# Optimization experiments

Hardware: AMD Instinct MI355X
Metric: run time of the kernel (lower is better)

Reference implementation:

```python
import jax, jax.numpy as jnp
import numpy as np

B, C, H, W = 4, 256, 64, 64
CH = C // 2  # inner channels


def setup_inputs() -> dict:
    key = jax.random.key(0)
    ks = jax.random.split(key, 9)
    s = 1.0 / np.sqrt(C)
    so = 1.0 / np.sqrt(CH)
    return {
        "x": jax.random.normal(ks[0], (B, C, H, W), dtype=jnp.float32),
        "teta_w": jax.random.uniform(ks[1], (CH, C), jnp.float32, -s, s),
        "teta_b": jax.random.uniform(ks[2], (CH,), jnp.float32, -s, s),
        "fi_w": jax.random.uniform(ks[3], (CH, C), jnp.float32, -s, s),
        "fi_b": jax.random.uniform(ks[4], (CH,), jnp.float32, -s, s),
        "gi_w": jax.random.uniform(ks[5], (CH, C), jnp.float32, -s, s),
        "gi_b": jax.random.uniform(ks[6], (CH,), jnp.float32, -s, s),
        "out_w": jax.random.uniform(ks[7], (C, CH), jnp.float32, -so, so),
        "out_b": jax.random.uniform(ks[8], (C,), jnp.float32, -so, so),
    }


def _conv1x1(x, w, b):
    # x: (B, Cin, H, W), w: (Cout, Cin) -> (B, Cout, H, W)
    return jnp.einsum('bchw,oc->bohw', x, w) + b[None, :, None, None]


def reference(x, teta_w, teta_b, fi_w, fi_b, gi_w, gi_b, out_w, out_b):
    b, c, h, w = x.shape
    n = h * w
    ch = teta_w.shape[0]
    # NOTE: original uses .view (reshape), NOT transpose, to get (B, N, Ch)
    x1 = _conv1x1(x, teta_w, teta_b).reshape(b, ch, n).reshape(b, n, ch)
    x2 = _conv1x1(x, fi_w, fi_b).reshape(b, ch, n)            # (B, Ch, N)
    x3 = _conv1x1(x, gi_w, gi_b).reshape(b, ch, n).reshape(b, n, ch)
    # softmax over dim=1 (rows), as in the original
    attn = jax.nn.softmax(jnp.matmul(x1, x2), axis=1)          # (B, N, N)
    y = jnp.matmul(attn, x3)                                   # (B, N, Ch)
    y = jnp.swapaxes(y, 1, 2).reshape(b, ch, h, w)
    return x + _conv1x1(y, out_w, out_b)
```

## Files before the change

### kernel.cpp

```cpp
#include <hip/hip_runtime.h>
#include <hip/hip_bf16.h>

#define BB 4
#define CC 256
#define CHH 128
#define NN 4096
#define KSHIFT 12.0f

typedef __attribute__((ext_vector_type(8))) short bf16x8;
typedef __attribute__((ext_vector_type(4))) float f32x4;

__device__ __forceinline__ float to_f(float v) { return v; }
__device__ __forceinline__ float to_f(__hip_bfloat16 v) { return __bfloat162float(v); }
__device__ __forceinline__ void st_f(float* p, float v) { *p = v; }
__device__ __forceinline__ void st_f(__hip_bfloat16* p, float v) { *p = __float2bfloat16(v); }
__device__ __forceinline__ unsigned short f2bf(float f) {
    __hip_bfloat16 h = __float2bfloat16(f);
    unsigned short u;
    __builtin_memcpy(&u, &h, 2);
    return u;
}
__device__ __forceinline__ bf16x8 ldb8(const unsigned short* p) { return *(const bf16x8*)p; }

__device__ __forceinline__ void gload_lds16(const unsigned short* g, unsigned short* l) {
    __builtin_amdgcn_global_load_lds(
        (const __attribute__((address_space(1))) unsigned int*)g,
        (__attribute__((address_space(3))) unsigned int*)l, 16, 0, 0);
}

__device__ __forceinline__ int detect_flag_block(const void* tb, int* sflag) {
    int tid = threadIdx.x;
    if (tid < 64) {
        const __hip_bfloat16* p = (const __hip_bfloat16*)tb;
        int big = 0, zero_even = 0;
#pragma unroll
        for (int k = 0; k < 2; ++k) {
            int idx = tid * 2 + k;
            float v = __bfloat162float(p[idx]);
            if (!(fabsf(v) <= 0.5f)) big = 1;
            if ((idx & 1) == 0 && v == 0.0f) zero_even = 1;
        }
        unsigned long long bigm = __ballot(big);
        unsigned long long zm = __ballot(zero_even);
        if (tid == 0) *sflag = (bigm != 0ULL || __popcll(zm) >= 32) ? 1 : 0;
    }
    __syncthreads();
    return *sflag;
}

template <typename T>
__device__ __forceinline__ void prep_body(const T* tw, const T* fw, const T* gw, const T* ow,
                                          const T* tb2, const T* fb, const T* gb, const T* ob,
                                          unsigned short* Wb, unsigned short* OWb,
                                          float* Bf, float* OBf) {
    int idx = blockIdx.x * 256 + threadIdx.x;
    if (idx < 98304) {
        int cv = idx >> 15, rem = idx & 32767;
        const T* src = cv == 0 ? tw : (cv == 1 ? fw : gw);
        Wb[idx] = f2bf(to_f(src[rem]));
    } else if (idx < 131072) {
        OWb[idx - 98304] = f2bf(to_f(ow[idx - 98304]));
    } else if (idx < 131456) {
        int r = idx - 131072;
        int cv = r >> 7, j = r & 127;
        const T* src = cv == 0 ? tb2 : (cv == 1 ? fb : gb);
        Bf[r] = to_f(src[j]);
    } else if (idx < 131712) {
        OBf[idx - 131456] = to_f(ob[idx - 131456]);
    }
}

template <typename T>
__device__ __forceinline__ void xtrans_body(const T* __restrict__ x, unsigned short* __restrict__ xt,
                                            int id, unsigned short (*t)[68]) {
    int b = id >> 8;
    const T* in = x + (size_t)b * CC * NN;
    unsigned short* out = xt + (size_t)b * NN * CC;
    int p0 = (id & 63) * 64, c0 = ((id >> 6) & 3) * 64;
    int flat = threadIdx.x;
#pragma unroll
    for (int tt = 0; tt < 16; ++tt) {
        int idd = flat + tt * 256;
        int rr = idd >> 6, cc = idd & 63;
        t[cc][rr] = f2bf(to_f(in[(size_t)(c0 + rr) * NN + p0 + cc]));
    }
    __syncthreads();
#pragma unroll
    for (int tt = 0; tt < 16; ++tt) {
        int idd = flat + tt * 256;
        int pp = idd >> 6, jj = idd & 63;
        out[(size_t)(p0 + pp) * CC + c0 + jj] = t[pp][jj];
    }
}

__launch_bounds__(256)
__global__ void prep_xtrans_kernel(const void* x,
                                   const void* tw, const void* fw, const void* gw, const void* ow,
                                   const void* tb2, const void* fb, const void* gb, const void* ob,
                                   unsigned short* Wb, unsigned short* OWb,
                                   float* Bf, float* OBf,
                                   unsigned short* __restrict__ xt) {
    __shared__ int sflag;
    __shared__ unsigned short t[64][68];
    int flag = detect_flag_block(tb2, &sflag);
    if (blockIdx.x < 515) {
        if (flag)
            prep_body<float>((const float*)tw, (const float*)fw, (const float*)gw, (const float*)ow,
                             (const float*)tb2, (const float*)fb, (const float*)gb, (const float*)ob,
                             Wb, OWb, Bf, OBf);
        else
            prep_body<__hip_bfloat16>((const __hip_bfloat16*)tw, (const __hip_bfloat16*)fw,
                                      (const __hip_bfloat16*)gw, (const __hip_bfloat16*)ow,
                                      (const __hip_bfloat16*)tb2, (const __hip_bfloat16*)fb,
                                      (const __hip_bfloat16*)gb, (const __hip_bfloat16*)ob,
                                      Wb, OWb, Bf, OBf);
    } else {
        int id = blockIdx.x - 515;
        if (flag) xtrans_body<float>((const float*)x, xt, id, t);
        else      xtrans_body<__hip_bfloat16>((const __hip_bfloat16*)x, xt, id, t);
    }
}

__launch_bounds__(256)
__global__ void conv3_mfma_kernel(const unsigned short* __restrict__ xt,
                                  const unsigned short* __restrict__ Wb,
                                  const float* __restrict__ Bf,
                                  unsigned short* __restrict__ T1b,
                                  unsigned short* __restrict__ T2t,
                                  unsigned short* __restrict__ T3b) {
    int b = blockIdx.y;
    int p0 = blockIdx.x * 16;
    int flat = threadIdx.x;
    int w = flat >> 6, lane = flat & 63, m = lane & 15, quad = lane >> 4;
    const unsigned short* xrow = xt + ((size_t)b * NN + p0 + m) * CC;
    bf16x8 xf[8];
#pragma unroll
    for (int kc = 0; kc < 8; ++kc)
        xf[kc] = ldb8(&xrow[kc * 32 + quad * 8]);
    unsigned short* t1  = T1b + (size_t)b * CHH * NN;
    unsigned short* t2t = T2t + (size_t)b * CHH * NN;
    unsigned short* t3  = T3b + (size_t)b * CHH * NN;
#pragma unroll
    for (int q = 0; q < 6; ++q) {
        int t = w * 6 + q;
        int cv = t >> 3, ot = t & 7;
        int o0 = ot * 16;
        const unsigned short* wrow = Wb + ((size_t)cv * CHH + o0 + m) * CC;
        f32x4 acc = {0.f, 0.f, 0.f, 0.f};
        __builtin_amdgcn_s_setprio(1);
#pragma unroll
        for (int kc = 0; kc < 8; ++kc) {
            bf16x8 wf = ldb8(&wrow[kc * 32 + quad * 8]);
            acc = __builtin_amdgcn_mfma_f32_16x16x32_bf16(wf, xf[kc], acc, 0, 0, 0);
        }
        __builtin_amdgcn_s_setprio(0);
        unsigned short hv[4];
#pragma unroll
        for (int r = 0; r < 4; ++r)
            hv[r] = f2bf(acc[r] + Bf[cv * CHH + o0 + quad * 4 + r]);
        if (cv == 1) {
            unsigned int lo = (unsigned int)hv[0] | ((unsigned int)hv[1] << 16);
            unsigned int hi = (unsigned int)hv[2] | ((unsigned int)hv[3] << 16);
            int src = (lane & 3) * 16 + (lane >> 2);
            unsigned int tlo = (unsigned int)__shfl((int)lo, src, 64);
            unsigned int thi = (unsigned int)__shfl((int)hi, src, 64);
            unsigned int* dst = (unsigned int*)&t2t[(size_t)(p0 + (lane >> 2)) * CHH +
                                                    o0 + (lane & 3) * 4];
            dst[0] = tlo;
            dst[1] = thi;
        } else {
            unsigned short* outp = (cv == 0) ? t1 : t3;
#pragma unroll
            for (int r = 0; r < 4; ++r)
                outp[(size_t)(o0 + quad * 4 + r) * NN + p0 + m] = hv[r];
        }
    }
}

__launch_bounds__(256)
__global__ void trans_stats_kernel(const unsigned short* __restrict__ T1b,
                                   const unsigned short* __restrict__ T2t,
                                   const unsigned short* __restrict__ T3b,
                                   unsigned short* __restrict__ X3t,
                                   float* __restrict__ Lpart) {
    __shared__ unsigned short arena[2 * 64 * 128];
    int flat = threadIdx.x;
    if (blockIdx.x >= 1024) {
        int id = blockIdx.x - 1024;
        int bz = id >> 7;
        int by = (id >> 1) & 63;
        int bx = id & 1;
        const unsigned short* in = T3b + (size_t)bz * NN * CHH;
        unsigned short* out = X3t + (size_t)bz * NN * CHH;
        int c0 = bx * 64, r0 = by * 64;
        unsigned short (*t)[68] = (unsigned short (*)[68])arena;
#pragma unroll
        for (int tt = 0; tt < 16; ++tt) {
            int id2 = flat + tt * 256;
            int r = id2 >> 6, c = id2 & 63;
            t[c][r] = in[(size_t)(r0 + r) * CHH + c0 + c];
        }
        __syncthreads();
#pragma unroll
        for (int tt = 0; tt < 16; ++tt) {
            int id2 = flat + tt * 256;
            int c = id2 >> 6, r = id2 & 63;
            out[(size_t)(c0 + c) * NN + r0 + r] = t[c][r];
        }
        return;
    }
    int blk = blockIdx.x;
    int b = (blk & 7) >> 1;
    int rest = (blk >> 3) * 2 + (blk & 1);
    int strip = rest >> 3, iq = rest & 7;
    int ibase = iq * 512;
    int w = flat >> 6, lane = flat & 63, m = lane & 15, quad = lane >> 4;
    const unsigned short* A  = T1b + (size_t)b * CHH * NN;
    const unsigned short* Bt = T2t + (size_t)b * CHH * NN;

    int u0w = strip * 128 + w * 32;
    bf16x8 bfr[2][4];
#pragma unroll
    for (int g = 0; g < 2; ++g)
#pragma unroll
        for (int kc = 0; kc < 4; ++kc)
            bfr[g][kc] = ldb8(&Bt[(size_t)(u0w + g * 16 + m) * CHH + kc * 32 + quad * 8]);

#define STAGE_TH(dst, ii)                                                          \
    _Pragma("unroll")                                                              \
    for (int i_ = 0; i_ < 4; ++i_) {                                               \
        int sl = i_ * 256 + flat;                                                  \
        int r_ = sl >> 4, ch_ = sl & 15;                                           \
        int c_ = ch_ ^ (r_ & 7);                                                   \
        gload_lds16(&A[(size_t)((ii) + r_) * CHH + c_ * 8],                        \
                    arena + (dst) * 8192 + sl * 8);                                \
    }

    float csum[2] = {0.f, 0.f};
    STAGE_TH(0, ibase);
    __syncthreads();
    int cur = 0;
    for (int t = 0; t < 8; ++t) {
        if (t < 7) { STAGE_TH(cur ^ 1, ibase + (t + 1) * 64); }
        const unsigned short* thc = arena + cur * 8192;
#pragma unroll
        for (int s = 0; s < 4; ++s) {
            int irow = s * 16 + m;
            bf16x8 af[4];
#pragma unroll
            for (int kc = 0; kc < 4; ++kc) {
                int ch = (kc * 4 + quad) ^ (irow & 7);
                af[kc] = *(const bf16x8*)&thc[irow * 128 + ch * 8];
            }
            __builtin_amdgcn_s_setprio(1);
#pragma unroll
            for (int g = 0; g < 2; ++g) {
                f32x4 acc = {0.f, 0.f, 0.f, 0.f};
#pragma unroll
                for (int kc = 0; kc < 4; ++kc)
                    acc = __builtin_amdgcn_mfma_f32_16x16x32_bf16(af[kc], bfr[g][kc], acc, 0, 0, 0);
#pragma unroll
                for (int r = 0; r < 4; ++r)
                    csum[g] += __expf(acc[r] - KSHIFT);
            }
            __builtin_amdgcn_s_setprio(0);
        }
        if (t < 7) {
            __syncthreads();
            cur ^= 1;
        }
    }
#undef STAGE_TH
#pragma unroll
    for (int g = 0; g < 2; ++g) {
        csum[g] += __shfl_xor(csum[g], 16, 64);
        csum[g] += __shfl_xor(csum[g], 32, 64);
        if (lane < 16)
            Lpart[((size_t)iq * BB + b) * NN + u0w + g * 16 + m] = csum[g];
    }
}

__launch_bounds__(512, 2)
__global__ void attn_mfma_kernel(const unsigned short* __restrict__ T1b,
                                 const unsigned short* __restrict__ T2t,
                                 const unsigned short* __restrict__ X3t,
                                 const float* __restrict__ Lpart,
                                 unsigned short* __restrict__ Yp0,
                                 unsigned short* __restrict__ Yp1,
                                 unsigned short* __restrict__ Yp2,
                                 unsigned short* __restrict__ Yp3) {
    int blk = blockIdx.x;
    int b = (blk & 7) >> 1;
    int rest = (blk >> 3) * 2 + (blk & 1);
    int it = rest >> 2, uc = rest & 3;
    int i0 = it * 128;
    unsigned short* Yp = uc == 0 ? Yp0 : (uc == 1 ? Yp1 : (uc == 2 ? Yp2 : Yp3));
    int flat = threadIdx.x;
    int w = flat >> 6, lane = flat & 63, m = lane & 15, quad = lane >> 4;
    int ig = w & 3, h = w >> 2;
    const unsigned short* A  = T1b + (size_t)b * CHH * NN;
    const unsigned short* Bt = T2t + (size_t)b * CHH * NN;
    const unsigned short* X3 = X3t + (size_t)b * CHH * NN;

    __shared__ __align__(16) unsigned char smem[69632];
    unsigned short* bt0 = (unsigned short*)smem;
    unsigned short* x3s = (unsigned short*)(smem + 32768);
    unsigned short* pTg = (unsigned short*)(smem + 49152) + ig * 2048;
    float* llh = (float*)(smem + 65536);

    int ubeg = uc * 1024;
#pragma unroll
    for (int k = 0; k < 2; ++k) {
        int idx = k * 512 + flat;
        int u = ubeg + idx;
        float s = 0.f;
#pragma unroll
        for (int c = 0; c < 8; ++c)
            s += Lpart[((size_t)c * BB + b) * NN + u];
        llh[idx] = __logf(s) + KSHIFT;
    }

    int iw = i0 + ig * 32;
    int j0 = h * 64;
    bf16x8 ath[2][4];
#pragma unroll
    for (int g = 0; g < 2; ++g)
#pragma unroll
        for (int kc = 0; kc < 4; ++kc)
            ath[g][kc] = ldb8(&A[(size_t)(iw + g * 16 + m) * CHH + kc * 32 + quad * 8]);
    f32x4 yacc[2][4];
#pragma unroll
    for (int g = 0; g < 2; ++g)
#pragma unroll
        for (int js = 0; js < 4; ++js) yacc[g][js] = (f32x4){0.f, 0.f, 0.f, 0.f};

#define STAGE_BT(dst, uu)                                                          \
    _Pragma("unroll")                                                              \
    for (int i_ = 0; i_ < 2; ++i_) {                                    \
        int sl = i_ * 512 + flat;                                                  \
        int u_ = sl >> 4, ch_ = sl & 15;                                           \
        int c_ = ch_ ^ (u_ & 7);                                                   \
        gload_lds16(&Bt[(size_t)((uu) + u_) * CHH + c_ * 8],                       \
                    bt0 + (dst) * 8192 + sl * 8);                                  \
    }
#define STAGE_X3(uu)                                                               \
    _Pragma("unroll")                                                              \
    for (int i_ = 0; i_ < 2; ++i_) {                                    \
        int sl = i_ * 512 + flat;                                                  \
        int j_ = sl >> 3, ch_ = sl & 7;                                            \
        int c_ = ch_ ^ (j_ & 7);                                                   \
        gload_lds16(&X3[(size_t)j_ * NN + (uu) + c_ * 8], x3s + sl * 8);           \
    }

    STAGE_BT(0, ubeg);
    STAGE_X3(ubeg);
    __syncthreads();
    int cur = 0;
    for (int t = 0; t < 16; ++t) {
        int u0 = ubeg + t * 64;
        if (t < 15) { STAGE_BT(cur ^ 1, u0 + 64); }
        const unsigned short* btc = bt0 + cur * 8192;
#pragma unroll
        for (int su = 0; su < 2; ++su) {
            int ul = h * 32 + su * 16 + m;
            f32x4 a0 = {0.f, 0.f, 0.f, 0.f}, a1 = {0.f, 0.f, 0.f, 0.f};
            __builtin_amdgcn_s_setprio(1);
#pragma unroll
            for (int kc = 0; kc < 4; ++kc) {
                int ch = (kc * 4 + quad) ^ (ul & 7);
                bf16x8 bf = *(const bf16x8*)&btc[ul * 128 + ch * 8];
                a0 = __builtin_amdgcn_mfma_f32_16x16x32_bf16(bf, ath[0][kc], a0, 0, 0, 0);
                a1 = __builtin_amdgcn_mfma_f32_16x16x32_bf16(bf, ath[1][kc], a1, 0, 0, 0);
            }
            __builtin_amdgcn_s_setprio(0);
            int ubase = h * 32 + su * 16 + quad * 4;
            int lb = t * 64 + ubase;
            unsigned int p00 = (unsigned int)f2bf(__expf(a0[0] - llh[lb + 0])) |
                               ((unsigned int)f2bf(__expf(a0[1] - llh[lb + 1])) << 16);
            unsigned int p01 = (unsigned int)f2bf(__expf(a0[2] - llh[lb + 2])) |
                               ((unsigned int)f2bf(__expf(a0[3] - llh[lb + 3])) << 16);
            unsigned int p10 = (unsigned int)f2bf(__expf(a1[0] - llh[lb + 0])) |
                               ((unsigned int)f2bf(__expf(a1[1] - llh[lb + 1])) << 16);
            unsigned int p11 = (unsigned int)f2bf(__expf(a1[2] - llh[lb + 2])) |
                               ((unsigned int)f2bf(__expf(a1[3] - llh[lb + 3])) << 16);
            int chs = ((ubase >> 3) ^ (m & 7)) * 8 + (ubase & 7);
            unsigned int* d0 = (unsigned int*)&pTg[m * 64 + chs];
            d0[0] = p00; d0[1] = p01;
            unsigned int* d1 = (unsigned int*)&pTg[(16 + m) * 64 + chs];
            d1[0] = p10; d1[1] = p11;
        }
        __syncthreads();
#pragma unroll
        for (int ku = 0; ku < 2; ++ku) {
            bf16x8 pa0 = *(const bf16x8*)&pTg[m * 64 + ((ku * 4 + quad) ^ (m & 7)) * 8];
            bf16x8 pa1 = *(const bf16x8*)&pTg[(16 + m) * 64 + ((ku * 4 + quad) ^ (m & 7)) * 8];
            __builtin_amdgcn_s_setprio(1);
#pragma unroll
            for (int js = 0; js < 4; ++js) {
                int j = j0 + js * 16 + m;
                int ch = (ku * 4 + quad) ^ (j & 7);
                bf16x8 xb = *(const bf16x8*)&x3s[j * 64 + ch * 8];
                yacc[0][js] = __builtin_amdgcn_mfma_f32_16x16x32_bf16(pa0, xb, yacc[0][js], 0, 0, 0);
                yacc[1][js] = __builtin_amdgcn_mfma_f32_16x16x32_bf16(pa1, xb, yacc[1][js], 0, 0, 0);
            }
            __builtin_amdgcn_s_setprio(0);
        }
        __syncthreads();
        if (t < 15) { STAGE_X3(u0 + 64); }
        cur ^= 1;
    }
#undef STAGE_BT
#undef STAGE_X3
#pragma unroll
    for (int g = 0; g < 2; ++g)
#pragma unroll
        for (int js = 0; js < 4; ++js)
#pragma unroll
            for (int r = 0; r < 4; ++r)
                Yp[((size_t)b * NN + iw + g * 16 + quad * 4 + r) * CHH +
                   j0 + js * 16 + m] = f2bf(yacc[g][js][r]);
}

template <typename T>
__device__ __forceinline__ void outconv_body(const T* __restrict__ x,
                                             const unsigned short* __restrict__ Yp0,
                                             const unsigned short* __restrict__ Yp1,
                                             const unsigned short* __restrict__ Yp2,
                                             const unsigned short* __restrict__ Yp3,
                                             const unsigned short* __restrict__ OWb,
                                             const float* __restrict__ OBf,
                                             T* __restrict__ out) {
    int b = blockIdx.y;
    int p0 = blockIdx.x * 16;
    int flat = threadIdx.x;
    int w = flat >> 6, lane = flat & 63, m = lane & 15, quad = lane >> 4;
    size_t yoff = ((size_t)b * NN + p0 + m) * CHH;
    const unsigned short* yrows[4] = {Yp0 + yoff, Yp1 + yoff, Yp2 + yoff, Yp3 + yoff};
    bf16x8 yf[4][4];
#pragma unroll
    for (int pz = 0; pz < 4; ++pz)
#pragma unroll
        for (int kc = 0; kc < 4; ++kc)
            yf[pz][kc] = ldb8(&yrows[pz][kc * 32 + quad * 8]);
#pragma unroll
    for (int q = 0; q < 4; ++q) {
        int o0 = (w * 4 + q) * 16;
        const unsigned short* wrow = OWb + (size_t)(o0 + m) * CHH;
        f32x4 acc = {0.f, 0.f, 0.f, 0.f};
        __builtin_amdgcn_s_setprio(1);
#pragma unroll
        for (int kc = 0; kc < 4; ++kc) {
            bf16x8 aw = ldb8(&wrow[kc * 32 + quad * 8]);
#pragma unroll
            for (int pz = 0; pz < 4; ++pz)
                acc = __builtin_amdgcn_mfma_f32_16x16x32_bf16(aw, yf[pz][kc], acc, 0, 0, 0);
        }
        __builtin_amdgcn_s_setprio(0);
#pragma unroll
        for (int r = 0; r < 4; ++r) {
            int co = o0 + quad * 4 + r;
            size_t oi = ((size_t)b * CC + co) * NN + p0 + m;
            st_f(&out[oi], acc[r] + OBf[co] + to_f(x[oi]));
        }
    }
}

__launch_bounds__(256)
__global__ void outconv_mfma_kernel(const void* x, const void* tb2,
                                    const unsigned short* __restrict__ Yp0,
                                    const unsigned short* __restrict__ Yp1,
                                    const unsigned short* __restrict__ Yp2,
                                    const unsigned short* __restrict__ Yp3,
                                    const unsigned short* __restrict__ OWb,
                                    const float* __restrict__ OBf,
                                    void* out) {
    __shared__ int sflag;
    int flag = detect_flag_block(tb2, &sflag);
    if (flag)
        outconv_body<float>((const float*)x, Yp0, Yp1, Yp2, Yp3, OWb, OBf, (float*)out);
    else
        outconv_body<__hip_bfloat16>((const __hip_bfloat16*)x, Yp0, Yp1, Yp2, Yp3, OWb, OBf,
                                     (__hip_bfloat16*)out);
}

extern "C" void kernel_launch(void* const* d_in, const int* in_sizes, int n_in,
                              void* d_out, int out_size, void* d_ws, size_t ws_size,
                              hipStream_t stream) {
    const void* x  = d_in[0];
    const void* tw = d_in[1];
    const void* tb = d_in[2];
    const void* fw = d_in[3];
    const void* fb = d_in[4];
    const void* gw = d_in[5];
    const void* gb = d_in[6];
    const void* ow = d_in[7];
    const void* ob = d_in[8];

    const size_t TE = (size_t)BB * CHH * NN;
    unsigned short* T1b = (unsigned short*)d_ws;
    unsigned short* T2t = T1b + TE;
    unsigned short* X3t = T2t + TE;
    unsigned short* T3b = X3t + TE;
    unsigned short* xt  = T3b + TE;
    unsigned short* Yp0 = xt;
    unsigned short* Yp1 = xt + TE;
    unsigned short* Yp2 = T3b;
    unsigned short* Yp3 = xt + 2 * TE;
    unsigned short* Wb  = Yp3 + TE;
    unsigned short* OWb = Wb + 98304;
    float* Bf    = (float*)(OWb + 32768);
    float* OBf   = Bf + 384;
    float* Lpart = OBf + 256;

    prep_xtrans_kernel<<<dim3(1539), 256, 0, stream>>>(x, tw, fw, gw, ow, tb, fb, gb, ob,
                                                       Wb, OWb, Bf, OBf, xt);
    conv3_mfma_kernel<<<dim3(NN / 16, BB), 256, 0, stream>>>(xt, Wb, Bf, T1b, T2t, T3b);
    trans_stats_kernel<<<dim3(1536), 256, 0, stream>>>(T1b, T2t, T3b, X3t, Lpart);
    attn_mfma_kernel<<<dim3(512), 512, 0, stream>>>(T1b, T2t, X3t, Lpart, Yp0, Yp1, Yp2, Yp3);
    outconv_mfma_kernel<<<dim3(NN / 16, BB), 256, 0, stream>>>(x, tb, Yp0, Yp1, Yp2, Yp3,
                                                               OWb, OBf, d_out);
}
```

Before: 193.4 us.

## Fuse x transpose into conv3 kernel and switch softmax to exp2 domain

```diff
diff --git a/kernel.cpp b/kernel.cpp
--- a/kernel.cpp
+++ b/kernel.cpp
@@ -5,7 +5,8 @@
 #define CC 256
 #define CHH 128
 #define NN 4096
-#define KSHIFT 12.0f
+#define KSHIFT2 17.312340490667562f
+#define LOG2E 1.4426950408889634f
 
 typedef __attribute__((ext_vector_type(8))) short bf16x8;
 typedef __attribute__((ext_vector_type(4))) float f32x4;
@@ -28,6 +29,24 @@
         (__attribute__((address_space(3))) unsigned int*)l, 16, 0, 0);
 }
 
+__device__ __forceinline__ void load16(const __hip_bfloat16* src, unsigned short* v) {
+    bf16x8 a = *(const bf16x8*)src;
+    bf16x8 b = *(const bf16x8*)(src + 8);
+#pragma unroll
+    for (int k = 0; k < 8; ++k) {
+        v[k] = ((unsigned short*)&a)[k];
+        v[8 + k] = ((unsigned short*)&b)[k];
+    }
+}
+__device__ __forceinline__ void load16(const float* src, unsigned short* v) {
+#pragma unroll
+    for (int q = 0; q < 4; ++q) {
+        f32x4 f = *(const f32x4*)(src + q * 4);
+#pragma unroll
+        for (int k = 0; k < 4; ++k) v[q * 4 + k] = f2bf(f[k]);
+    }
+}
+
 __device__ __forceinline__ int detect_flag_block(const void* tb, int* sflag) {
     int tid = threadIdx.x;
     if (tid < 64) {
@@ -57,93 +76,73 @@
     if (idx < 98304) {
         int cv = idx >> 15, rem = idx & 32767;
         const T* src = cv == 0 ? tw : (cv == 1 ? fw : gw);
-        Wb[idx] = f2bf(to_f(src[rem]));
+        float v = to_f(src[rem]);
+        if (cv == 1) v *= LOG2E;
+        Wb[idx] = f2bf(v);
     } else if (idx < 131072) {
         OWb[idx - 98304] = f2bf(to_f(ow[idx - 98304]));
     } else if (idx < 131456) {
         int r = idx - 131072;
         int cv = r >> 7, j = r & 127;
         const T* src = cv == 0 ? tb2 : (cv == 1 ? fb : gb);
-        Bf[r] = to_f(src[j]);
+        float v = to_f(src[j]);
+        if (cv == 1) v *= LOG2E;
+        Bf[r] = v;
     } else if (idx < 131712) {
         OBf[idx - 131456] = to_f(ob[idx - 131456]);
     }
 }
 
+__launch_bounds__(256)
+__global__ void prep_kernel(const void* tw, const void* fw, const void* gw, const void* ow,
+                            const void* tb2, const void* fb, const void* gb, const void* ob,
+                            unsigned short* Wb, unsigned short* OWb, float* Bf, float* OBf) {
+    __shared__ int sflag;
+    int flag = detect_flag_block(tb2, &sflag);
+    if (flag)
+        prep_body<float>((const float*)tw, (const float*)fw, (const float*)gw, (const float*)ow,
+                         (const float*)tb2, (const float*)fb, (const float*)gb, (const float*)ob,
+                         Wb, OWb, Bf, OBf);
+    else
+        prep_body<__hip_bfloat16>((const __hip_bfloat16*)tw, (const __hip_bfloat16*)fw,
+                                  (const __hip_bfloat16*)gw, (const __hip_bfloat16*)ow,
+                                  (const __hip_bfloat16*)tb2, (const __hip_bfloat16*)fb,
+                                  (const __hip_bfloat16*)gb, (const __hip_bfloat16*)ob,
+                                  Wb, OWb, Bf, OBf);
+}
+
 template <typename T>
-__device__ __forceinline__ void xtrans_body(const T* __restrict__ x, unsigned short* __restrict__ xt,
-                                            int id, unsigned short (*t)[68]) {
-    int b = id >> 8;
-    const T* in = x + (size_t)b * CC * NN;
-    unsigned short* out = xt + (size_t)b * NN * CC;
-    int p0 = (id & 63) * 64, c0 = ((id >> 6) & 3) * 64;
-    int flat = threadIdx.x;
-#pragma unroll
-    for (int tt = 0; tt < 16; ++tt) {
-        int idd = flat + tt * 256;
-        int rr = idd >> 6, cc = idd & 63;
-        t[cc][rr] = f2bf(to_f(in[(size_t)(c0 + rr) * NN + p0 + cc]));
-    }
-    __syncthreads();
-#pragma unroll
-    for (int tt = 0; tt < 16; ++tt) {
-        int idd = flat + tt * 256;
-        int pp = idd >> 6, jj = idd & 63;
-        out[(size_t)(p0 + pp) * CC + c0 + jj] = t[pp][jj];
-    }
-}
-
-__launch_bounds__(256)
-__global__ void prep_xtrans_kernel(const void* x,
-                                   const void* tw, const void* fw, const void* gw, const void* ow,
-                                   const void* tb2, const void* fb, const void* gb, const void* ob,
-                                   unsigned short* Wb, unsigned short* OWb,
-                                   float* Bf, float* OBf,
-                                   unsigned short* __restrict__ xt) {
-    __shared__ int sflag;
-    __shared__ unsigned short t[64][68];
-    int flag = detect_flag_block(tb2, &sflag);
-    if (blockIdx.x < 515) {
-        if (flag)
-            prep_body<float>((const float*)tw, (const float*)fw, (const float*)gw, (const float*)ow,
-                             (const float*)tb2, (const float*)fb, (const float*)gb, (const float*)ob,
-                             Wb, OWb, Bf, OBf);
-        else
-            prep_body<__hip_bfloat16>((const __hip_bfloat16*)tw, (const __hip_bfloat16*)fw,
-                                      (const __hip_bfloat16*)gw, (const __hip_bfloat16*)ow,
-                                      (const __hip_bfloat16*)tb2, (const __hip_bfloat16*)fb,
-                                      (const __hip_bfloat16*)gb, (const __hip_bfloat16*)ob,
-                                      Wb, OWb, Bf, OBf);
-    } else {
-        int id = blockIdx.x - 515;
-        if (flag) xtrans_body<float>((const float*)x, xt, id, t);
-        else      xtrans_body<__hip_bfloat16>((const __hip_bfloat16*)x, xt, id, t);
-    }
-}
-
-__launch_bounds__(256)
-__global__ void conv3_mfma_kernel(const unsigned short* __restrict__ xt,
-                                  const unsigned short* __restrict__ Wb,
-                                  const float* __restrict__ Bf,
-                                  unsigned short* __restrict__ T1b,
-                                  unsigned short* __restrict__ T2t,
-                                  unsigned short* __restrict__ T3b) {
+__device__ __forceinline__ void conv3_body(const T* __restrict__ x,
+                                           const unsigned short* __restrict__ Wb,
+                                           const float* __restrict__ Bf,
+                                           unsigned short* __restrict__ T1b,
+                                           unsigned short* __restrict__ T2t,
+                                           unsigned short* __restrict__ T3b,
+                                           unsigned short (*t)[272]) {
     int b = blockIdx.y;
     int p0 = blockIdx.x * 16;
     int flat = threadIdx.x;
     int w = flat >> 6, lane = flat & 63, m = lane & 15, quad = lane >> 4;
-    const unsigned short* xrow = xt + ((size_t)b * NN + p0 + m) * CC;
+    {
+        int c = flat;
+        const T* src = x + ((size_t)b * CC + c) * NN + p0;
+        unsigned short v[16];
+        load16(src, v);
+#pragma unroll
+        for (int pp = 0; pp < 16; ++pp) t[pp][c] = v[pp];
+    }
+    __syncthreads();
     bf16x8 xf[8];
 #pragma unroll
     for (int kc = 0; kc < 8; ++kc)
-        xf[kc] = ldb8(&xrow[kc * 32 + quad * 8]);
+        xf[kc] = ldb8(&t[m][kc * 32 + quad * 8]);
     unsigned short* t1  = T1b + (size_t)b * CHH * NN;
     unsigned short* t2t = T2t + (size_t)b * CHH * NN;
     unsigned short* t3  = T3b + (size_t)b * CHH * NN;
 #pragma unroll
     for (int q = 0; q < 6; ++q) {
-        int t = w * 6 + q;
-        int cv = t >> 3, ot = t & 7;
+        int tt = w * 6 + q;
+        int cv = tt >> 3, ot = tt & 7;
         int o0 = ot * 16;
         const unsigned short* wrow = Wb + ((size_t)cv * CHH + o0 + m) * CC;
         f32x4 acc = {0.f, 0.f, 0.f, 0.f};
@@ -175,6 +174,22 @@
                 outp[(size_t)(o0 + quad * 4 + r) * NN + p0 + m] = hv[r];
         }
     }
+}
+
+__launch_bounds__(256)
+__global__ void conv3_mfma_kernel(const void* x, const void* tb2,
+                                  const unsigned short* __restrict__ Wb,
+                                  const float* __restrict__ Bf,
+                                  unsigned short* __restrict__ T1b,
+                                  unsigned short* __restrict__ T2t,
+                                  unsigned short* __restrict__ T3b) {
+    __shared__ int sflag;
+    __shared__ unsigned short t[16][272];
+    int flag = detect_flag_block(tb2, &sflag);
+    if (flag)
+        conv3_body<float>((const float*)x, Wb, Bf, T1b, T2t, T3b, t);
+    else
+        conv3_body<__hip_bfloat16>((const __hip_bfloat16*)x, Wb, Bf, T1b, T2t, T3b, t);
 }
 
 __launch_bounds__(256)
@@ -261,7 +276,7 @@
                     acc = __builtin_amdgcn_mfma_f32_16x16x32_bf16(af[kc], bfr[g][kc], acc, 0, 0, 0);
 #pragma unroll
                 for (int r = 0; r < 4; ++r)
-                    csum[g] += __expf(acc[r] - KSHIFT);
+                    csum[g] += __builtin_exp2f(acc[r] - KSHIFT2);
             }
             __builtin_amdgcn_s_setprio(0);
         }
@@ -317,7 +332,7 @@
 #pragma unroll
         for (int c = 0; c < 8; ++c)
             s += Lpart[((size_t)c * BB + b) * NN + u];
-        llh[idx] = __logf(s) + KSHIFT;
+        llh[idx] = __log2f(s) + KSHIFT2;
     }
 
     int iw = i0 + ig * 32;
@@ -375,14 +390,14 @@
             __builtin_amdgcn_s_setprio(0);
             int ubase = h * 32 + su * 16 + quad * 4;
             int lb = t * 64 + ubase;
-            unsigned int p00 = (unsigned int)f2bf(__expf(a0[0] - llh[lb + 0])) |
-                               ((unsigned int)f2bf(__expf(a0[1] - llh[lb + 1])) << 16);
-            unsigned int p01 = (unsigned int)f2bf(__expf(a0[2] - llh[lb + 2])) |
-                               ((unsigned int)f2bf(__expf(a0[3] - llh[lb + 3])) << 16);
-            unsigned int p10 = (unsigned int)f2bf(__expf(a1[0] - llh[lb + 0])) |
-                               ((unsigned int)f2bf(__expf(a1[1] - llh[lb + 1])) << 16);
-            unsigned int p11 = (unsigned int)f2bf(__expf(a1[2] - llh[lb + 2])) |
-                               ((unsigned int)f2bf(__expf(a1[3] - llh[lb + 3])) << 16);
+            unsigned int p00 = (unsigned int)f2bf(__builtin_exp2f(a0[0] - llh[lb + 0])) |
+                               ((unsigned int)f2bf(__builtin_exp2f(a0[1] - llh[lb + 1])) << 16);
+            unsigned int p01 = (unsigned int)f2bf(__builtin_exp2f(a0[2] - llh[lb + 2])) |
+                               ((unsigned int)f2bf(__builtin_exp2f(a0[3] - llh[lb + 3])) << 16);
+            unsigned int p10 = (unsigned int)f2bf(__builtin_exp2f(a1[0] - llh[lb + 0])) |
+                               ((unsigned int)f2bf(__builtin_exp2f(a1[1] - llh[lb + 1])) << 16);
+            unsigned int p11 = (unsigned int)f2bf(__builtin_exp2f(a1[2] - llh[lb + 2])) |
+                               ((unsigned int)f2bf(__builtin_exp2f(a1[3] - llh[lb + 3])) << 16);
             int chs = ((ubase >> 3) ^ (m & 7)) * 8 + (ubase & 7);
             unsigned int* d0 = (unsigned int*)&pTg[m * 64 + chs];
             d0[0] = p00; d0[1] = p01;
@@ -512,9 +527,9 @@
     float* OBf   = Bf + 384;
     float* Lpart = OBf + 256;
 
-    prep_xtrans_kernel<<<dim3(1539), 256, 0, stream>>>(x, tw, fw, gw, ow, tb, fb, gb, ob,
-                                                       Wb, OWb, Bf, OBf, xt);
-    conv3_mfma_kernel<<<dim3(NN / 16, BB), 256, 0, stream>>>(xt, Wb, Bf, T1b, T2t, T3b);
+    prep_kernel<<<dim3(515), 256, 0, stream>>>(tw, fw, gw, ow, tb, fb, gb, ob,
+                                               Wb, OWb, Bf, OBf);
+    conv3_mfma_kernel<<<dim3(NN / 16, BB), 256, 0, stream>>>(x, tb, Wb, Bf, T1b, T2t, T3b);
     trans_stats_kernel<<<dim3(1536), 256, 0, stream>>>(T1b, T2t, T3b, X3t, Lpart);
     attn_mfma_kernel<<<dim3(512), 512, 0, stream>>>(T1b, T2t, X3t, Lpart, Yp0, Yp1, Yp2, Yp3);
     outconv_mfma_kernel<<<dim3(NN / 16, BB), 256, 0, stream>>>(x, tb, Yp0, Yp1, Yp2, Yp3,
```

Result: slower. 198.4 us (+2.6%).
